# Performance work log

Hardware: AMD Instinct MI355X
Metric: run time of the kernel (lower is better)

## Reference

```python
import jax, jax.numpy as jnp
import numpy as np
from jax import lax

NUM_LAYERS = 2
H = 1024   # per-direction hidden = state_size / 2
IN = 768   # BERT hidden size == input_size
SEQ = 1024


def _init_params(key):
    ks = jax.random.split(key, 4 * NUM_LAYERS * 2)
    mk = lambda k, shape: jax.random.normal(k, shape, jnp.float32) * 0.02
    out = {}
    i = 0
    for d in ("fw", "bw"):
        for l in range(NUM_LAYERS):
            ins = IN if l == 0 else H
            out[f"{d}{l}_Wih"] = mk(ks[i], (4 * H, ins)); i += 1
            out[f"{d}{l}_Whh"] = mk(ks[i], (4 * H, H)); i += 1
            out[f"{d}{l}_bih"] = mk(ks[i], (4 * H,)); i += 1
            out[f"{d}{l}_bhh"] = mk(ks[i], (4 * H,)); i += 1
    return out


def setup_inputs() -> dict:
    key = jax.random.key(0)
    kx, kp = jax.random.split(key)
    inp = {"last_hidden": jax.random.normal(kx, (1, SEQ, IN), jnp.float32)}
    inp.update(_init_params(kp))
    return inp


def _run_direction(x, params):
    """x: [S, in_dim]; params: list of (Wih, Whh, bih, bhh) per layer.
    Stacked LSTMCells (torch gate order i,f,g,o), dropout_amount=0."""
    def step(carry, xt):
        new = []
        inp = xt
        for (h, c), (Wih, Whh, bih, bhh) in zip(carry, params):
            gates = Wih @ inp + bih + Whh @ h + bhh  # [4H]
            i, f, g, o = jnp.split(gates, 4)
            c = jax.nn.sigmoid(f) * c + jax.nn.sigmoid(i) * jnp.tanh(g)
            h = jax.nn.sigmoid(o) * jnp.tanh(c)
            new.append((h, c))
            inp = h
        return tuple(new), inp  # output = top layer h
    init = tuple((jnp.zeros((H,), x.dtype), jnp.zeros((H,), x.dtype)) for _ in params)
    final, outs = lax.scan(step, init, x)
    cs = jnp.stack([c for (_, c) in final])  # [L, H] final cell states
    hs = jnp.stack([h for (h, _) in final])  # [L, H] final hidden states
    return cs, hs, outs                      # outs: [S, H]


def reference(last_hidden, fw0_Wih, fw0_Whh, fw0_bih, fw0_bhh,
              fw1_Wih, fw1_Whh, fw1_bih, fw1_bhh,
              bw0_Wih, bw0_Whh, bw0_bih, bw0_bhh,
              bw1_Wih, bw1_Whh, bw1_bih, bw1_bhh):
    x = last_hidden[0]  # squeeze batch of 1 -> [S, IN]
    fw = [(fw0_Wih, fw0_Whh, fw0_bih, fw0_bhh), (fw1_Wih, fw1_Whh, fw1_bih, fw1_bhh)]
    bw = [(bw0_Wih, bw0_Whh, bw0_bih, bw0_bhh), (bw1_Wih, bw1_Whh, bw1_bih, bw1_bhh)]
    f_c, f_h, f_out = _run_direction(x, fw)
    b_c, b_h, b_out = _run_direction(x[::-1], bw)
    b_out = b_out[::-1]  # re-align backward outputs with token order
    cell_memories = jnp.concatenate([f_c, b_c], axis=1)      # [L, 2H]
    hidden_states = jnp.concatenate([f_h, b_h], axis=1)      # [L, 2H]
    final_outputs = jnp.concatenate([f_out, b_out], axis=1)  # [S, 2H]
    return cell_memories, hidden_states, final_outputs
```

## Files before the change

kernel.cpp:

```cpp
#include <hip/hip_runtime.h>

typedef unsigned int u32;
typedef unsigned short u16;
typedef unsigned long long u64;
typedef __attribute__((ext_vector_type(8))) short v8s;
typedef __attribute__((ext_vector_type(4))) float v4f;

#define VALIDMASK 0x0001000100010001ULL

__device__ __forceinline__ float bf2f(u16 v) { return __uint_as_float(((u32)v) << 16); }
__device__ __forceinline__ u16 f2bf(float f) {
    u32 u = __float_as_uint(f);
    return (u16)((u + 0x7fffu + ((u >> 16) & 1u)) >> 16);
}
__device__ __forceinline__ u32 f2bfo(float f) { return (__float_as_uint(f) >> 16) | 1u; }
__device__ __forceinline__ float sigf(float x) { return 1.0f / (1.0f + __expf(-x)); }
__device__ __forceinline__ float tanhfast(float x) {
    float e = __expf(2.0f * x);
    return 1.0f - 2.0f / (e + 1.0f);
}
__device__ __forceinline__ v8s pack8(v4f a, v4f b) {
    v8s r;
    r[0] = (short)f2bf(a[0]); r[1] = (short)f2bf(a[1]);
    r[2] = (short)f2bf(a[2]); r[3] = (short)f2bf(a[3]);
    r[4] = (short)f2bf(b[0]); r[5] = (short)f2bf(b[1]);
    r[6] = (short)f2bf(b[2]); r[7] = (short)f2bf(b[3]);
    return r;
}

__global__ __launch_bounds__(256) void gemm_ih(
    const float* __restrict__ A, const float* __restrict__ W,
    const float* __restrict__ bih, const float* __restrict__ bhh,
    u16* __restrict__ out, int K)
{
    __shared__ u16 As[128][40];
    __shared__ u16 Bs[128][40];
    const int tm = blockIdx.x, tn = blockIdx.y;
    const int tid = threadIdx.x;
    const int lane = tid & 63;
    const int wv = tid >> 6;
    const int wm = wv >> 1, wn = wv & 1;
    const int fr = lane & 15, fq = lane >> 4;

    v4f acc[4][4] = {};

    for (int kt = 0; kt < K; kt += 32) {
#pragma unroll
        for (int it = 0; it < 2; ++it) {
            int q = tid + it * 256;
            int r = q >> 2;
            int c8 = (q & 3) * 8;
            const float* pa = &A[(size_t)(tm * 128 + r) * K + kt + c8];
            const float* pw = &W[(size_t)(tn * 128 + r) * K + kt + c8];
            *(v8s*)&As[r][c8] = pack8(*(const v4f*)pa, *(const v4f*)(pa + 4));
            *(v8s*)&Bs[r][c8] = pack8(*(const v4f*)pw, *(const v4f*)(pw + 4));
        }
        __syncthreads();
        v8s af[4], bfr[4];
#pragma unroll
        for (int mi = 0; mi < 4; ++mi)
            af[mi] = *(const v8s*)&As[wm * 64 + mi * 16 + fr][fq * 8];
#pragma unroll
        for (int ni = 0; ni < 4; ++ni)
            bfr[ni] = *(const v8s*)&Bs[wn * 64 + ni * 16 + fr][fq * 8];
#pragma unroll
        for (int mi = 0; mi < 4; ++mi)
#pragma unroll
            for (int ni = 0; ni < 4; ++ni)
                acc[mi][ni] = __builtin_amdgcn_mfma_f32_16x16x32_bf16(af[mi], bfr[ni], acc[mi][ni], 0, 0, 0);
        __syncthreads();
    }

#pragma unroll
    for (int ni = 0; ni < 4; ++ni) {
        int col = tn * 128 + wn * 64 + ni * 16 + fr;
        float bias = bih[col] + bhh[col];
#pragma unroll
        for (int mi = 0; mi < 4; ++mi)
#pragma unroll
            for (int j = 0; j < 4; ++j) {
                int row = tm * 128 + wm * 64 + mi * 16 + fq * 4 + j;
                out[(size_t)row * 4096 + col] = f2bf(acc[mi][ni][j] + bias);
            }
    }
}

__global__ __launch_bounds__(64, 1) void lstm_fused(
    const float* __restrict__ fw0_Whh, const float* __restrict__ bw0_Whh,
    const float* __restrict__ fw1_Whh, const float* __restrict__ bw1_Whh,
    const float* __restrict__ fw1_Wih, const float* __restrict__ bw1_Wih,
    const float* __restrict__ fw1_bih, const float* __restrict__ fw1_bhh,
    const float* __restrict__ bw1_bih, const float* __restrict__ bw1_bhh,
    const u16*  __restrict__ precomp0,
    u64* htag0,
    u64* htag1,
    float* __restrict__ out)
{
    extern __shared__ char smem[];
    char* hA = smem + 65536;
    char* hB = smem + 65536 + 2048;
    float* gd = (float*)(smem + 65536 + 4096);

    const int lane = threadIdx.x;
    const int bid = blockIdx.x;
    const int role = bid >> 8;
    const int sub = bid & 255;
    const int d = sub >> 7;
    const int wg = sub & 127;
    const int e0 = wg << 3;
    const int q16 = (lane >> 4) << 4;

    const float* __restrict__ Whh =
        role ? (d ? bw1_Whh : fw1_Whh) : (d ? bw0_Whh : fw0_Whh);

    v8s awf0[32], awf1[32];
    {
        int r0 = lane & 15, r1 = r0 + 16;
        int kq = (lane >> 4) << 3;
        const float* p0 = &Whh[(size_t)((r0 >> 3) * 1024 + e0 + (r0 & 7)) * 1024 + kq];
        const float* p1 = &Whh[(size_t)((r1 >> 3) * 1024 + e0 + (r1 & 7)) * 1024 + kq];
#pragma unroll
        for (int c = 0; c < 32; ++c) {
            awf0[c] = pack8(*(const v4f*)(p0 + 32 * c), *(const v4f*)(p0 + 32 * c + 4));
            awf1[c] = pack8(*(const v4f*)(p1 + 32 * c), *(const v4f*)(p1 + 32 * c + 4));
        }
    }

    float bias_i = 0.f, bias_f = 0.f, bias_g = 0.f, bias_o = 0.f;
    if (role) {
        const float* __restrict__ Wih = d ? bw1_Wih : fw1_Wih;
        for (int i = 0; i < 32; ++i) {
            const float* prow = &Wih[(size_t)((i >> 3) * 1024 + e0 + (i & 7)) * 1024];
            int base = ((lane & 3) << 9) + ((i >> 4) << 8) + ((i & 15) << 4);
            const float* p0 = prow + lane * 8;
            const float* p1 = prow + 512 + lane * 8;
            *(v8s*)(smem + ((lane >> 2) << 11) + base) =
                pack8(*(const v4f*)p0, *(const v4f*)(p0 + 4));
            *(v8s*)(smem + ((16 + (lane >> 2)) << 11) + base) =
                pack8(*(const v4f*)p1, *(const v4f*)(p1 + 4));
        }
        if (lane < 8) {
            const float* bi = d ? bw1_bih : fw1_bih;
            const float* bh = d ? bw1_bhh : fw1_bhh;
            bias_i = bi[e0 + lane]        + bh[e0 + lane];
            bias_f = bi[1024 + e0 + lane] + bh[1024 + e0 + lane];
            bias_g = bi[2048 + e0 + lane] + bh[2048 + e0 + lane];
            bias_o = bi[3072 + e0 + lane] + bh[3072 + e0 + lane];
        }
    }

    u64* hown = (role ? htag1 : htag0) + (size_t)d * 1024 * 256;
    u64* hin  = htag0 + (size_t)d * 1024 * 256;
    float* cm_out = out + role * 2048;
    float* hs_out = out + 4096 + role * 2048;
    float* seq_out = out + 8192;

    float c_state = 0.0f;

    for (int s = 0; s < 1024; ++s) {
        v4f acc0a = {0.f,0.f,0.f,0.f}, acc0b = {0.f,0.f,0.f,0.f};
        v4f acc1a = {0.f,0.f,0.f,0.f}, acc1b = {0.f,0.f,0.f,0.f};

        u16 ri = 0, rf = 0, rg = 0, ro = 0;
        if (!role && lane < 8) {
            int sx = d ? (1023 - s) : s;
            const u16* pr = precomp0 + ((size_t)d * 1024 + sx) * 4096 + e0 + lane;
            ri = pr[0]; rf = pr[1024]; rg = pr[2048]; ro = pr[3072];
        }

        if (role) {
            u64* p = hin + (size_t)s * 256 + lane;
            u64 a, b, c2, d2;
            for (;;) {
                a  = __hip_atomic_load(&p[0],   __ATOMIC_RELAXED, __HIP_MEMORY_SCOPE_AGENT);
                b  = __hip_atomic_load(&p[64],  __ATOMIC_RELAXED, __HIP_MEMORY_SCOPE_AGENT);
                c2 = __hip_atomic_load(&p[128], __ATOMIC_RELAXED, __HIP_MEMORY_SCOPE_AGENT);
                d2 = __hip_atomic_load(&p[192], __ATOMIC_RELAXED, __HIP_MEMORY_SCOPE_AGENT);
                if ((((a & b) & (c2 & d2)) & VALIDMASK) == VALIDMASK) break;
                __builtin_amdgcn_s_sleep(1);
            }
            __builtin_amdgcn_s_setprio(1);
            *(u64*)(hB + (lane << 3))        = a;
            *(u64*)(hB + (lane << 3) + 512)  = b;
            *(u64*)(hB + (lane << 3) + 1024) = c2;
            *(u64*)(hB + (lane << 3) + 1536) = d2;
            asm volatile("s_waitcnt lgkmcnt(0)" ::: "memory");
            const int fb = ((lane >> 4) << 9) + ((lane & 15) << 4);
#pragma unroll
            for (int c = 0; c < 32; c += 2) {
                v8s b0 = *(const v8s*)(hB + (c << 6) + q16);
                v8s b1 = *(const v8s*)(hB + ((c + 1) << 6) + q16);
                v8s a00 = *(const v8s*)(smem + (c << 11) + fb);
                v8s a01 = *(const v8s*)(smem + (c << 11) + fb + 256);
                v8s a10 = *(const v8s*)(smem + ((c + 1) << 11) + fb);
                v8s a11 = *(const v8s*)(smem + ((c + 1) << 11) + fb + 256);
                acc0a = __builtin_amdgcn_mfma_f32_16x16x32_bf16(a00, b0, acc0a, 0, 0, 0);
                acc1a = __builtin_amdgcn_mfma_f32_16x16x32_bf16(a01, b0, acc1a, 0, 0, 0);
                acc0b = __builtin_amdgcn_mfma_f32_16x16x32_bf16(a10, b1, acc0b, 0, 0, 0);
                acc1b = __builtin_amdgcn_mfma_f32_16x16x32_bf16(a11, b1, acc1b, 0, 0, 0);
            }
            __builtin_amdgcn_s_setprio(0);
        }

        if (s > 0) {
            u64* p = hown + (size_t)(s - 1) * 256 + lane;
            u64 a, b, c2, d2;
            for (;;) {
                a  = __hip_atomic_load(&p[0],   __ATOMIC_RELAXED, __HIP_MEMORY_SCOPE_AGENT);
                b  = __hip_atomic_load(&p[64],  __ATOMIC_RELAXED, __HIP_MEMORY_SCOPE_AGENT);
                c2 = __hip_atomic_load(&p[128], __ATOMIC_RELAXED, __HIP_MEMORY_SCOPE_AGENT);
                d2 = __hip_atomic_load(&p[192], __ATOMIC_RELAXED, __HIP_MEMORY_SCOPE_AGENT);
                if ((((a & b) & (c2 & d2)) & VALIDMASK) == VALIDMASK) break;
                __builtin_amdgcn_s_sleep(1);
            }
            __builtin_amdgcn_s_setprio(1);
            *(u64*)(hA + (lane << 3))        = a;
            *(u64*)(hA + (lane << 3) + 512)  = b;
            *(u64*)(hA + (lane << 3) + 1024) = c2;
            *(u64*)(hA + (lane << 3) + 1536) = d2;
            asm volatile("s_waitcnt lgkmcnt(0)" ::: "memory");
#pragma unroll
            for (int c = 0; c < 32; c += 2) {
                v8s b0 = *(const v8s*)(hA + (c << 6) + q16);
                v8s b1 = *(const v8s*)(hA + ((c + 1) << 6) + q16);
                acc0a = __builtin_amdgcn_mfma_f32_16x16x32_bf16(awf0[c], b0, acc0a, 0, 0, 0);
                acc1a = __builtin_amdgcn_mfma_f32_16x16x32_bf16(awf1[c], b0, acc1a, 0, 0, 0);
                acc0b = __builtin_amdgcn_mfma_f32_16x16x32_bf16(awf0[c + 1], b1, acc0b, 0, 0, 0);
                acc1b = __builtin_amdgcn_mfma_f32_16x16x32_bf16(awf1[c + 1], b1, acc1b, 0, 0, 0);
            }
            __builtin_amdgcn_s_setprio(0);
        }

        v4f acc0 = acc0a + acc0b;
        v4f acc1 = acc1a + acc1b;
        if ((lane & 15) == 0) {
            int rbase = (lane >> 4) << 2;
            *(v4f*)&gd[rbase]      = acc0;
            *(v4f*)&gd[16 + rbase] = acc1;
        }
        asm volatile("s_waitcnt lgkmcnt(0)" ::: "memory");

        float h_new = 0.0f;
        if (lane < 8) {
            float Gi = gd[lane]      + (role ? bias_i : bf2f(ri));
            float Gf = gd[8 + lane]  + (role ? bias_f : bf2f(rf));
            float Gg = gd[16 + lane] + (role ? bias_g : bf2f(rg));
            float Go = gd[24 + lane] + (role ? bias_o : bf2f(ro));
            c_state = sigf(Gf) * c_state + sigf(Gi) * tanhfast(Gg);
            h_new = sigf(Go) * tanhfast(c_state);
        }

        u32 w0 = f2bfo(__shfl(h_new, (lane << 2)))     | (f2bfo(__shfl(h_new, (lane << 2) + 1)) << 16);
        u32 w1 = f2bfo(__shfl(h_new, (lane << 2) + 2)) | (f2bfo(__shfl(h_new, (lane << 2) + 3)) << 16);
        if (lane < 2) {
            u64 val = ((u64)w1 << 32) | w0;
            __hip_atomic_store(&hown[(size_t)s * 256 + (e0 >> 2) + lane], val,
                               __ATOMIC_RELAXED, __HIP_MEMORY_SCOPE_AGENT);
        }

        if (lane < 8) {
            if (role) {
                int rrow = d ? (1023 - s) : s;
                seq_out[(size_t)rrow * 2048 + d * 1024 + e0 + lane] = h_new;
            }
            if (s == 1023) {
                cm_out[d * 1024 + e0 + lane] = c_state;
                hs_out[d * 1024 + e0 + lane] = h_new;
            }
        }
    }
}

extern "C" void kernel_launch(void* const* d_in, const int* in_sizes, int n_in,
                              void* d_out, int out_size, void* d_ws, size_t ws_size,
                              hipStream_t stream) {
    (void)in_sizes; (void)n_in; (void)out_size; (void)ws_size;

    const float* x       = (const float*)d_in[0];
    const float* fw0_Wih = (const float*)d_in[1];
    const float* fw0_Whh = (const float*)d_in[2];
    const float* fw0_bih = (const float*)d_in[3];
    const float* fw0_bhh = (const float*)d_in[4];
    const float* fw1_Wih = (const float*)d_in[5];
    const float* fw1_Whh = (const float*)d_in[6];
    const float* fw1_bih = (const float*)d_in[7];
    const float* fw1_bhh = (const float*)d_in[8];
    const float* bw0_Wih = (const float*)d_in[9];
    const float* bw0_Whh = (const float*)d_in[10];
    const float* bw0_bih = (const float*)d_in[11];
    const float* bw0_bhh = (const float*)d_in[12];
    const float* bw1_Wih = (const float*)d_in[13];
    const float* bw1_Whh = (const float*)d_in[14];
    const float* bw1_bih = (const float*)d_in[15];
    const float* bw1_bhh = (const float*)d_in[16];

    char* ws = (char*)d_ws;
    u16* precomp = (u16*)ws;
    u64* htag0   = (u64*)(ws + (16 << 20));
    u64* htag1   = (u64*)(ws + (20 << 20));
    float* out   = (float*)d_out;

    hipMemsetAsync(htag0, 0, (size_t)8 << 20, stream);

    dim3 g(8, 32);
    gemm_ih<<<g, 256, 0, stream>>>(x, fw0_Wih, fw0_bih, fw0_bhh, precomp, 768);
    gemm_ih<<<g, 256, 0, stream>>>(x, bw0_Wih, bw0_bih, bw0_bhh,
                                   precomp + (size_t)1024 * 4096, 768);

    lstm_fused<<<512, 64, 69760, stream>>>(
        fw0_Whh, bw0_Whh, fw1_Whh, bw1_Whh, fw1_Wih, bw1_Wih,
        fw1_bih, fw1_bhh, bw1_bih, bw1_bhh,
        precomp, htag0, htag1, out);
}
```

Baseline: 3.623 ms.

## Software-pipeline layer-1 input projection to the step after publishing h

For the layer-1 role, the Wih·h0 product for step s+1 now runs at the end of step s, after this block's own h has been published, instead of at the start of step s+1. The input-side MFMA work is taken off the critical path between receiving the block's own previous h and computing the next gates. In exchange, the accumulator chain for the prefetched product is serialized into two accumulators instead of four, and the setprio hints around it are dropped.

Result: faster. 3.222 ms (-11.1%).

```diff
diff --git a/kernel.cpp b/kernel.cpp
--- a/kernel.cpp
+++ b/kernel.cpp
@@ -156,6 +156,39 @@
     float* seq_out = out + 8192;
 
     float c_state = 0.0f;
+    v4f wacc0 = {0.f,0.f,0.f,0.f}, wacc1 = {0.f,0.f,0.f,0.f};
+    const int fb = ((lane >> 4) << 9) + ((lane & 15) << 4);
+
+    if (role) {
+        u64* p = hin + lane;
+        u64 a, b, c2, d2;
+        for (;;) {
+            a  = __hip_atomic_load(&p[0],   __ATOMIC_RELAXED, __HIP_MEMORY_SCOPE_AGENT);
+            b  = __hip_atomic_load(&p[64],  __ATOMIC_RELAXED, __HIP_MEMORY_SCOPE_AGENT);
+            c2 = __hip_atomic_load(&p[128], __ATOMIC_RELAXED, __HIP_MEMORY_SCOPE_AGENT);
+            d2 = __hip_atomic_load(&p[192], __ATOMIC_RELAXED, __HIP_MEMORY_SCOPE_AGENT);
+            if ((((a & b) & (c2 & d2)) & VALIDMASK) == VALIDMASK) break;
+            __builtin_amdgcn_s_sleep(1);
+        }
+        *(u64*)(hB + (lane << 3))        = a;
+        *(u64*)(hB + (lane << 3) + 512)  = b;
+        *(u64*)(hB + (lane << 3) + 1024) = c2;
+        *(u64*)(hB + (lane << 3) + 1536) = d2;
+        asm volatile("s_waitcnt lgkmcnt(0)" ::: "memory");
+#pragma unroll
+        for (int c = 0; c < 32; c += 2) {
+            v8s b0 = *(const v8s*)(hB + (c << 6) + q16);
+            v8s b1 = *(const v8s*)(hB + ((c + 1) << 6) + q16);
+            v8s a00 = *(const v8s*)(smem + (c << 11) + fb);
+            v8s a01 = *(const v8s*)(smem + (c << 11) + fb + 256);
+            v8s a10 = *(const v8s*)(smem + ((c + 1) << 11) + fb);
+            v8s a11 = *(const v8s*)(smem + ((c + 1) << 11) + fb + 256);
+            wacc0 = __builtin_amdgcn_mfma_f32_16x16x32_bf16(a00, b0, wacc0, 0, 0, 0);
+            wacc1 = __builtin_amdgcn_mfma_f32_16x16x32_bf16(a01, b0, wacc1, 0, 0, 0);
+            wacc0 = __builtin_amdgcn_mfma_f32_16x16x32_bf16(a10, b1, wacc0, 0, 0, 0);
+            wacc1 = __builtin_amdgcn_mfma_f32_16x16x32_bf16(a11, b1, wacc1, 0, 0, 0);
+        }
+    }
 
     for (int s = 0; s < 1024; ++s) {
         v4f acc0a = {0.f,0.f,0.f,0.f}, acc0b = {0.f,0.f,0.f,0.f};
@@ -166,40 +199,6 @@
             int sx = d ? (1023 - s) : s;
             const u16* pr = precomp0 + ((size_t)d * 1024 + sx) * 4096 + e0 + lane;
             ri = pr[0]; rf = pr[1024]; rg = pr[2048]; ro = pr[3072];
-        }
-
-        if (role) {
-            u64* p = hin + (size_t)s * 256 + lane;
-            u64 a, b, c2, d2;
-            for (;;) {
-                a  = __hip_atomic_load(&p[0],   __ATOMIC_RELAXED, __HIP_MEMORY_SCOPE_AGENT);
-                b  = __hip_atomic_load(&p[64],  __ATOMIC_RELAXED, __HIP_MEMORY_SCOPE_AGENT);
-                c2 = __hip_atomic_load(&p[128], __ATOMIC_RELAXED, __HIP_MEMORY_SCOPE_AGENT);
-                d2 = __hip_atomic_load(&p[192], __ATOMIC_RELAXED, __HIP_MEMORY_SCOPE_AGENT);
-                if ((((a & b) & (c2 & d2)) & VALIDMASK) == VALIDMASK) break;
-                __builtin_amdgcn_s_sleep(1);
-            }
-            __builtin_amdgcn_s_setprio(1);
-            *(u64*)(hB + (lane << 3))        = a;
-            *(u64*)(hB + (lane << 3) + 512)  = b;
-            *(u64*)(hB + (lane << 3) + 1024) = c2;
-            *(u64*)(hB + (lane << 3) + 1536) = d2;
-            asm volatile("s_waitcnt lgkmcnt(0)" ::: "memory");
-            const int fb = ((lane >> 4) << 9) + ((lane & 15) << 4);
-#pragma unroll
-            for (int c = 0; c < 32; c += 2) {
-                v8s b0 = *(const v8s*)(hB + (c << 6) + q16);
-                v8s b1 = *(const v8s*)(hB + ((c + 1) << 6) + q16);
-                v8s a00 = *(const v8s*)(smem + (c << 11) + fb);
-                v8s a01 = *(const v8s*)(smem + (c << 11) + fb + 256);
-                v8s a10 = *(const v8s*)(smem + ((c + 1) << 11) + fb);
-                v8s a11 = *(const v8s*)(smem + ((c + 1) << 11) + fb + 256);
-                acc0a = __builtin_amdgcn_mfma_f32_16x16x32_bf16(a00, b0, acc0a, 0, 0, 0);
-                acc1a = __builtin_amdgcn_mfma_f32_16x16x32_bf16(a01, b0, acc1a, 0, 0, 0);
-                acc0b = __builtin_amdgcn_mfma_f32_16x16x32_bf16(a10, b1, acc0b, 0, 0, 0);
-                acc1b = __builtin_amdgcn_mfma_f32_16x16x32_bf16(a11, b1, acc1b, 0, 0, 0);
-            }
-            __builtin_amdgcn_s_setprio(0);
         }
 
         if (s > 0) {
@@ -231,8 +230,8 @@
             __builtin_amdgcn_s_setprio(0);
         }
 
-        v4f acc0 = acc0a + acc0b;
-        v4f acc1 = acc1a + acc1b;
+        v4f acc0 = acc0a + acc0b + wacc0;
+        v4f acc1 = acc1a + acc1b + wacc1;
         if ((lane & 15) == 0) {
             int rbase = (lane >> 4) << 2;
             *(v4f*)&gd[rbase]      = acc0;
@@ -266,6 +265,39 @@
             if (s == 1023) {
                 cm_out[d * 1024 + e0 + lane] = c_state;
                 hs_out[d * 1024 + e0 + lane] = h_new;
+            }
+        }
+
+        if (role && s < 1023) {
+            wacc0 = (v4f){0.f,0.f,0.f,0.f};
+            wacc1 = (v4f){0.f,0.f,0.f,0.f};
+            u64* p = hin + (size_t)(s + 1) * 256 + lane;
+            u64 a, b, c2, d2;
+            for (;;) {
+                a  = __hip_atomic_load(&p[0],   __ATOMIC_RELAXED, __HIP_MEMORY_SCOPE_AGENT);
+                b  = __hip_atomic_load(&p[64],  __ATOMIC_RELAXED, __HIP_MEMORY_SCOPE_AGENT);
+                c2 = __hip_atomic_load(&p[128], __ATOMIC_RELAXED, __HIP_MEMORY_SCOPE_AGENT);
+                d2 = __hip_atomic_load(&p[192], __ATOMIC_RELAXED, __HIP_MEMORY_SCOPE_AGENT);
+                if ((((a & b) & (c2 & d2)) & VALIDMASK) == VALIDMASK) break;
+                __builtin_amdgcn_s_sleep(1);
+            }
+            *(u64*)(hB + (lane << 3))        = a;
+            *(u64*)(hB + (lane << 3) + 512)  = b;
+            *(u64*)(hB + (lane << 3) + 1024) = c2;
+            *(u64*)(hB + (lane << 3) + 1536) = d2;
+            asm volatile("s_waitcnt lgkmcnt(0)" ::: "memory");
+#pragma unroll
+            for (int c = 0; c < 32; c += 2) {
+                v8s b0 = *(const v8s*)(hB + (c << 6) + q16);
+                v8s b1 = *(const v8s*)(hB + ((c + 1) << 6) + q16);
+                v8s a00 = *(const v8s*)(smem + (c << 11) + fb);
+                v8s a01 = *(const v8s*)(smem + (c << 11) + fb + 256);
+                v8s a10 = *(const v8s*)(smem + ((c + 1) << 11) + fb);
+                v8s a11 = *(const v8s*)(smem + ((c + 1) << 11) + fb + 256);
+                wacc0 = __builtin_amdgcn_mfma_f32_16x16x32_bf16(a00, b0, wacc0, 0, 0, 0);
+                wacc1 = __builtin_amdgcn_mfma_f32_16x16x32_bf16(a01, b0, wacc1, 0, 0, 0);
+                wacc0 = __builtin_amdgcn_mfma_f32_16x16x32_bf16(a10, b1, wacc0, 0, 0, 0);
+                wacc1 = __builtin_amdgcn_mfma_f32_16x16x32_bf16(a11, b1, wacc1, 0, 0, 0);
             }
         }
     }
```
